# Kernel tuning notes

Measured on AMD Instinct MI355X. Metric: run time of the kernel, lower is better.

Reference implementation:

```python
import jax, jax.numpy as jnp
import numpy as np

NORMALIZED_LENGTH = 1.0
LOSS_WEIGHTS = (0.25, 1.0)
EPS = 1e-12  # matches torch F.normalize eps


def setup_inputs() -> dict:
    key = jax.random.key(0)
    k1, k2 = jax.random.split(key)
    x = jax.random.normal(k1, (16, 128, 64, 64), dtype=jnp.float32)
    codebook = jax.random.normal(k2, (1024, 128), dtype=jnp.float32)
    return {"x": x, "codebook": codebook}


def _forward(x, codebook):
    # --- VQCodebook.forward: normalize x along channel dim (dim=1) ---
    # NOTE: the torch source's codebook renormalization uses non-in-place
    # .div/.mul whose results are discarded, so the codebook is unchanged.
    if NORMALIZED_LENGTH > 0:
        nrm = jnp.linalg.norm(x, axis=1, keepdims=True)  # [B,1,H,W]
        x = NORMALIZED_LENGTH * x / jnp.maximum(nrm, EPS)

    B, C, H, W = x.shape
    z = jnp.transpose(x, (0, 2, 3, 1)).reshape(-1, C)  # [N, C], N = B*H*W

    # Pairwise squared L2 distances via ||z||^2 - 2 z c^T + ||c||^2.
    # argmin of squared distance == argmin of distance.
    z2 = jnp.sum(z * z, axis=1, keepdims=True)             # [N, 1]
    c2 = jnp.sum(codebook * codebook, axis=1)              # [K]
    d2 = z2 - 2.0 * jnp.einsum('nc,kc->nk', z, codebook) + c2[None, :]  # [N, K]
    idx = jnp.argmin(d2, axis=1)                           # [N]

    q = codebook[idx]                                      # [N, C]
    q = q.reshape(B, H, W, C).transpose(0, 3, 1, 2)        # [B, C, H, W]

    lw0, lw1 = LOSS_WEIGHTS
    diff_codebook = jax.lax.stop_gradient(x) - q
    diff_commit = x - jax.lax.stop_gradient(q)
    loss0 = lw0 * jnp.mean(jnp.linalg.norm(diff_codebook, axis=1))
    loss1 = lw1 * jnp.mean(jnp.linalg.norm(diff_commit, axis=1))
    return q, loss0, loss1


def reference(x, codebook):
    return _forward(x, codebook)
```

## Files before the change

### kernel.cpp

```cpp
#include <hip/hip_runtime.h>
#include <math.h>

#define K_CODES 1024
#define C_DIM   128
#define HW      4096
#define CHW     (C_DIM*HW)
#define N_POS   65536
#define Q_ELEMS 8388608

#define WS_S    0
#define WS_C2   256
#define WS_IDX  8192


typedef __attribute__((ext_vector_type(8))) short short8;
typedef __attribute__((ext_vector_type(4))) float f32x4;

__device__ __forceinline__ unsigned short f2bf(float f) {
    unsigned u = __float_as_uint(f);
    u += 0x7FFFu + ((u >> 16) & 1u);
    return (unsigned short)(u >> 16);
}

__device__ __forceinline__ void gll16(const void* g, void* l) {
    __builtin_amdgcn_global_load_lds(
        (const __attribute__((address_space(1))) void*)g,
        (__attribute__((address_space(3))) void*)l, 16, 0, 0);
}

__global__ void prep_kernel(const float* __restrict__ cb, float* __restrict__ ws,
                            unsigned short* __restrict__ cbbf) {
    __shared__ __align__(16) unsigned short srow[128];
    int k = blockIdx.x;
    int l = threadIdx.x;
    if (k == 0 && l == 0) *(float*)((char*)ws + WS_S) = 0.f;
    float v1 = cb[k * C_DIM + l];
    float v2 = cb[k * C_DIM + 64 + l];
    int c1 = l, c2 = 64 + l;
    srow[(((c1 >> 3) ^ (k & 7)) << 3) | (c1 & 7)] = f2bf(v1);
    srow[(((c2 >> 3) ^ (k & 7)) << 3) | (c2 & 7)] = f2bf(v2);
    float ss = v1 * v1 + v2 * v2;
    #pragma unroll
    for (int off = 32; off > 0; off >>= 1) ss += __shfl_down(ss, off);
    if (l == 0) ((float*)((char*)ws + WS_C2))[k] = ss;
    __syncthreads();
    if (l < 16) ((uint4*)cbbf)[k * 16 + l] = ((const uint4*)srow)[l];
}

__global__ __launch_bounds__(256, 2) void vq_mfma(const float* __restrict__ x,
                                                  const float* __restrict__ cb,
                                                  const unsigned short* __restrict__ cbbf,
                                                  const float* __restrict__ c2w,
                                                  int* __restrict__ idxw,
                                                  float* __restrict__ Sw,
                                                  float* __restrict__ out) {
    __shared__ __align__(16) unsigned short cbuf[2 * 1024 * 8];
    __shared__ float mbuf[2][2][16][3];
    __shared__ int ibuf[64];

    const int t  = threadIdx.x;
    const int w  = t >> 6;
    const int kh = w & 1;
    const int pg = w >> 1;
    const int ln = t & 63;
    const int lp = ln & 15;
    const int q  = ln >> 4;
    const int bid = blockIdx.x;
    const int b   = bid >> 6;
    const int s0  = (bid & 63) << 6;

    short8 xf[2][4];
    float  r2v[2];
    {
        float ss[2] = {0.f, 0.f};
        #pragma unroll
        for (int pt = 0; pt < 2; ++pt) {
            const float* xgp = x + b * CHW + s0 + pg * 32 + pt * 16 + lp;
            #pragma unroll
            for (int cs = 0; cs < 4; ++cs) {
                union { short8 v; unsigned short u[8]; } fu;
                #pragma unroll
                for (int j = 0; j < 8; ++j) {
                    float vv = xgp[(32 * cs + 8 * q + j) * HW];
                    ss[pt] = fmaf(vv, vv, ss[pt]);
                    fu.u[j] = f2bf(vv);
                }
                xf[pt][cs] = fu.v;
            }
        }
        #pragma unroll
        for (int pt = 0; pt < 2; ++pt) {
            float s = ss[pt];
            s += __shfl_xor(s, 16);
            s += __shfl_xor(s, 32);
            r2v[pt] = -2.0f / fmaxf(sqrtf(s), 1e-12f);
        }
    }

    const float FMAX = __uint_as_float(0x7F7FFFFFu);
    float m1[2] = {FMAX, FMAX}, m2[2] = {FMAX, FMAX}, m3[2] = {FMAX, FMAX};

    const char* gbase = (const char*)cbbf + (kh * 512) * 256 + (pg * 512 + ln) * 16;
    char* lbase = (char*)cbuf + (kh * 1024 + pg * 512) * 16;

    #pragma unroll
    for (int r = 0; r < 8; ++r)
        gll16(gbase + r * 1024, lbase + r * 1024);
    __syncthreads();

    for (int i = 0; i < 8; ++i) {
        const int k0 = kh * 512 + i * 64;

        f32x4 acc[4][2];
        #pragma unroll
        for (int ct = 0; ct < 4; ++ct)
            #pragma unroll
            for (int pt = 0; pt < 2; ++pt) acc[ct][pt] = 0;

        const unsigned short* cbp = cbuf + kh * 8192;
        #pragma unroll
        for (int cs = 0; cs < 4; ++cs) {
            short8 ah[4];
            #pragma unroll
            for (int ct = 0; ct < 4; ++ct) {
                int g = (16 * ct + lp) * 16 + ((4 * cs + q) ^ (lp & 7));
                ah[ct] = *(const short8*)(cbp + g * 8);
            }
            #pragma unroll
            for (int ct = 0; ct < 4; ++ct)
                #pragma unroll
                for (int pt = 0; pt < 2; ++pt)
                    acc[ct][pt] = __builtin_amdgcn_mfma_f32_16x16x32_bf16(
                        ah[ct], xf[pt][cs], acc[ct][pt], 0, 0, 0);
        }

        #pragma unroll
        for (int ct = 0; ct < 4; ++ct) {
            float4 c2vv = *(const float4*)(c2w + k0 + 16 * ct + 4 * q);
            float c2a[4] = {c2vv.x, c2vv.y, c2vv.z, c2vv.w};
            const int kb0 = k0 + 16 * ct + 4 * q;
            #pragma unroll
            for (int pt = 0; pt < 2; ++pt) {
                #pragma unroll
                for (int reg = 0; reg < 4; ++reg) {
                    float s = fmaf(r2v[pt], acc[ct][pt][reg], c2a[reg]);
                    unsigned pb = (__float_as_uint(s) & 0xFFFFFC00u) |
                                  (unsigned)(kb0 + reg);
                    float u  = __uint_as_float(pb);
                    float t3 = __builtin_amdgcn_fmed3f(m2[pt], m3[pt], u);
                    float t2 = __builtin_amdgcn_fmed3f(m1[pt], m2[pt], u);
                    m1[pt] = fminf(m1[pt], u); m2[pt] = t2; m3[pt] = t3;
                }
            }
        }

        if (i < 7) {
            __syncthreads();
            #pragma unroll
            for (int r = 0; r < 8; ++r)
                gll16(gbase + (i + 1) * 16384 + r * 1024, lbase + r * 1024);
            __syncthreads();
        }
    }

    #pragma unroll
    for (int d = 16; d <= 32; d <<= 1) {
        #pragma unroll
        for (int pt = 0; pt < 2; ++pt) {
            float o1 = __shfl_xor(m1[pt], d), o2 = __shfl_xor(m2[pt], d),
                  o3 = __shfl_xor(m3[pt], d);
            float u, t2, t3;
            u = o1; t3 = __builtin_amdgcn_fmed3f(m2[pt], m3[pt], u);
            t2 = __builtin_amdgcn_fmed3f(m1[pt], m2[pt], u);
            m1[pt] = fminf(m1[pt], u); m2[pt] = t2; m3[pt] = t3;
            u = o2; t3 = __builtin_amdgcn_fmed3f(m2[pt], m3[pt], u);
            t2 = __builtin_amdgcn_fmed3f(m1[pt], m2[pt], u);
            m1[pt] = fminf(m1[pt], u); m2[pt] = t2; m3[pt] = t3;
            u = o3; t3 = __builtin_amdgcn_fmed3f(m2[pt], m3[pt], u);
            t2 = __builtin_amdgcn_fmed3f(m1[pt], m2[pt], u);
            m1[pt] = fminf(m1[pt], u); m2[pt] = t2; m3[pt] = t3;
        }
    }

    if (kh == 1 && ln < 16) {
        #pragma unroll
        for (int pt = 0; pt < 2; ++pt) {
            mbuf[pg][pt][lp][0] = m1[pt];
            mbuf[pg][pt][lp][1] = m2[pt];
            mbuf[pg][pt][lp][2] = m3[pt];
        }
    }
    __syncthreads();

    if (kh == 0) {
        float lsum = 0.f;
        #pragma unroll
        for (int pt = 0; pt < 2; ++pt) {
            #pragma unroll
            for (int c = 0; c < 3; ++c) {
                float u  = mbuf[pg][pt][lp][c];
                float t3 = __builtin_amdgcn_fmed3f(m2[pt], m3[pt], u);
                float t2 = __builtin_amdgcn_fmed3f(m1[pt], m2[pt], u);
                m1[pt] = fminf(m1[pt], u); m2[pt] = t2; m3[pt] = t3;
            }
            int ks[3] = {(int)(__float_as_uint(m1[pt]) & 1023u),
                         (int)(__float_as_uint(m2[pt]) & 1023u),
                         (int)(__float_as_uint(m3[pt]) & 1023u)};

            float xr[32];
            const float* xgp = x + b * CHW + s0 + pg * 32 + pt * 16 + lp;
            #pragma unroll
            for (int cs = 0; cs < 4; ++cs)
                #pragma unroll
                for (int j = 0; j < 8; ++j)
                    xr[cs * 8 + j] = xgp[(32 * cs + 8 * q + j) * HW];

            float dots[3];
            #pragma unroll
            for (int jj = 0; jj < 3; ++jj) {
                const float* crow = cb + ks[jj] * C_DIM + 8 * q;
                float p = 0.f;
                #pragma unroll
                for (int cs = 0; cs < 4; ++cs) {
                    float4 a0 = *(const float4*)(crow + 32 * cs);
                    float4 a1 = *(const float4*)(crow + 32 * cs + 4);
                    p = fmaf(xr[cs*8+0], a0.x, p); p = fmaf(xr[cs*8+1], a0.y, p);
                    p = fmaf(xr[cs*8+2], a0.z, p); p = fmaf(xr[cs*8+3], a0.w, p);
                    p = fmaf(xr[cs*8+4], a1.x, p); p = fmaf(xr[cs*8+5], a1.y, p);
                    p = fmaf(xr[cs*8+6], a1.z, p); p = fmaf(xr[cs*8+7], a1.w, p);
                }
                p += __shfl_xor(p, 16);
                p += __shfl_xor(p, 32);
                dots[jj] = p;
            }
            float sb = fmaf(r2v[pt], dots[0], c2w[ks[0]]); int kb = ks[0];
            float s2 = fmaf(r2v[pt], dots[1], c2w[ks[1]]);
            if (s2 < sb || (s2 == sb && ks[1] < kb)) { sb = s2; kb = ks[1]; }
            float s3 = fmaf(r2v[pt], dots[2], c2w[ks[2]]);
            if (s3 < sb || (s3 == sb && ks[2] < kb)) { sb = s3; kb = ks[2]; }

            if (ln < 16) {
                idxw[bid * 64 + pg * 32 + pt * 16 + lp] = kb;
                ibuf[pg * 32 + pt * 16 + lp] = kb;
            }
            lsum += sqrtf(fmaxf(1.0f + sb, 0.f));
        }
        #pragma unroll
        for (int off = 32; off > 0; off >>= 1) lsum += __shfl_down(lsum, off);
        if (ln == 0) atomicAdd(Sw, 0.25f * lsum);
    }

    __syncthreads();
    if (b != 0) {
        const int row = ibuf[ln];
        const float4* cbr = (const float4*)cb + row * 32;
        float* ob = out + b * CHW + s0 + ln;
        #pragma unroll
        for (int c4 = w * 8; c4 < w * 8 + 8; ++c4) {
            float4 v = cbr[c4];
            float* o = ob + (c4 * 4) * HW;
            o[0]      = v.x;
            o[HW]     = v.y;
            o[2 * HW] = v.z;
            o[3 * HW] = v.w;
        }
    }
}

__global__ void write_q0(const float* __restrict__ cb,
                         const int* __restrict__ idxw,
                         const float* __restrict__ ws,
                         float* __restrict__ out) {
    int id = blockIdx.x * 256 + threadIdx.x;
    int s  = id & 4095;
    int c4 = id >> 12;
    int row = idxw[s];
    float4 v = ((const float4*)cb)[row * 32 + c4];
    float* o = out + (c4 * 4) * HW + s;
    o[0]      = v.x;
    o[HW]     = v.y;
    o[2 * HW] = v.z;
    o[3 * HW] = v.w;
    if (id == 0) {
        float S = *(const float*)((const char*)ws + WS_S);
        float m = S / (float)N_POS;
        out[Q_ELEMS]     = 0.25f * m;
        out[Q_ELEMS + 1] = m;
    }
}

extern "C" void kernel_launch(void* const* d_in, const int* in_sizes, int n_in,
                              void* d_out, int out_size, void* d_ws, size_t ws_size,
                              hipStream_t stream) {
    const float* x  = (const float*)d_in[0];
    const float* cb = (const float*)d_in[1];
    float* out = (float*)d_out;
    float* ws  = (float*)d_ws;

    const float* c2w = (const float*)((const char*)d_ws + WS_C2);
    int*  idxw = (int*)((char*)d_ws + WS_IDX);
    float* Sw  = (float*)((char*)d_ws + WS_S);
    unsigned short* cbbf = (unsigned short*)d_out;

    prep_kernel<<<K_CODES, 64, 0, stream>>>(cb, ws, cbbf);
    vq_mfma    <<<N_POS / 64, 256, 0, stream>>>(x, cb, cbbf, c2w, idxw, Sw, out);
    write_q0   <<<512, 256, 0, stream>>>(cb, idxw, ws, out);
}
```

Measured before the change: 70.66 us.

## Give each wave a private codebook quarter with double-buffered async loads

Each of the four waves now owns a 256-code slice of the codebook and processes all 64 positions, rather than splitting codes in halves and positions in pairs. Each wave streams its slice through its own double-buffered LDS region and synchronises with s_waitcnt alone, so block-wide __syncthreads are gone and the next chunk's load overlaps the current MFMA work. The top-3 merge now reduces candidates from four waves through LDS. The cost is more registers for x fragments and accumulators (4 position tiles per wave), which may reduce occupancy, plus each wave re-reading and converting all of x.

```diff
diff --git a/kernel.cpp b/kernel.cpp
--- a/kernel.cpp
+++ b/kernel.cpp
@@ -54,14 +54,12 @@
                                                   int* __restrict__ idxw,
                                                   float* __restrict__ Sw,
                                                   float* __restrict__ out) {
-    __shared__ __align__(16) unsigned short cbuf[2 * 1024 * 8];
-    __shared__ float mbuf[2][2][16][3];
+    __shared__ __align__(16) unsigned short cbuf[2][4][4096];
+    __shared__ float mbuf[4][4][16][3];
     __shared__ int ibuf[64];
 
     const int t  = threadIdx.x;
     const int w  = t >> 6;
-    const int kh = w & 1;
-    const int pg = w >> 1;
     const int ln = t & 63;
     const int lp = ln & 15;
     const int q  = ln >> 4;
@@ -69,13 +67,23 @@
     const int b   = bid >> 6;
     const int s0  = (bid & 63) << 6;
 
-    short8 xf[2][4];
-    float  r2v[2];
+    const char* gq = (const char*)cbbf + (w << 16);
+
     {
-        float ss[2] = {0.f, 0.f};
-        #pragma unroll
-        for (int pt = 0; pt < 2; ++pt) {
-            const float* xgp = x + b * CHW + s0 + pg * 32 + pt * 16 + lp;
+        const char* gs = gq + (ln << 4);
+        char* ld = (char*)&cbuf[0][w][0];
+        #pragma unroll
+        for (int r = 0; r < 8; ++r) gll16(gs + r * 1024, ld + r * 1024);
+    }
+
+    short8 xf[4][4];
+    float  r2v[4];
+    {
+        float ss[4];
+        #pragma unroll
+        for (int pt = 0; pt < 4; ++pt) {
+            ss[pt] = 0.f;
+            const float* xgp = x + b * CHW + s0 + pt * 16 + lp;
             #pragma unroll
             for (int cs = 0; cs < 4; ++cs) {
                 union { short8 v; unsigned short u[8]; } fu;
@@ -89,7 +97,7 @@
             }
         }
         #pragma unroll
-        for (int pt = 0; pt < 2; ++pt) {
+        for (int pt = 0; pt < 4; ++pt) {
             float s = ss[pt];
             s += __shfl_xor(s, 16);
             s += __shfl_xor(s, 32);
@@ -98,49 +106,54 @@
     }
 
     const float FMAX = __uint_as_float(0x7F7FFFFFu);
-    float m1[2] = {FMAX, FMAX}, m2[2] = {FMAX, FMAX}, m3[2] = {FMAX, FMAX};
-
-    const char* gbase = (const char*)cbbf + (kh * 512) * 256 + (pg * 512 + ln) * 16;
-    char* lbase = (char*)cbuf + (kh * 1024 + pg * 512) * 16;
-
-    #pragma unroll
-    for (int r = 0; r < 8; ++r)
-        gll16(gbase + r * 1024, lbase + r * 1024);
-    __syncthreads();
+    float m1[4] = {FMAX, FMAX, FMAX, FMAX};
+    float m2[4] = {FMAX, FMAX, FMAX, FMAX};
+    float m3[4] = {FMAX, FMAX, FMAX, FMAX};
+
+    asm volatile("s_waitcnt vmcnt(0)" ::: "memory");
+    __builtin_amdgcn_sched_barrier(0);
 
     for (int i = 0; i < 8; ++i) {
-        const int k0 = kh * 512 + i * 64;
-
-        f32x4 acc[4][2];
-        #pragma unroll
-        for (int ct = 0; ct < 4; ++ct)
-            #pragma unroll
-            for (int pt = 0; pt < 2; ++pt) acc[ct][pt] = 0;
-
-        const unsigned short* cbp = cbuf + kh * 8192;
+        if (i < 7) {
+            asm volatile("s_waitcnt lgkmcnt(0)" ::: "memory");
+            const char* gs = gq + (i + 1) * 8192 + (ln << 4);
+            char* ld = (char*)&cbuf[(i + 1) & 1][w][0];
+            #pragma unroll
+            for (int r = 0; r < 8; ++r) gll16(gs + r * 1024, ld + r * 1024);
+        }
+
+        const int k0 = (w << 8) + (i << 5);
+        const unsigned short* cbp = &cbuf[i & 1][w][0];
+
+        f32x4 acc[2][4];
+        #pragma unroll
+        for (int ct = 0; ct < 2; ++ct)
+            #pragma unroll
+            for (int pt = 0; pt < 4; ++pt) acc[ct][pt] = 0;
+
         #pragma unroll
         for (int cs = 0; cs < 4; ++cs) {
-            short8 ah[4];
-            #pragma unroll
-            for (int ct = 0; ct < 4; ++ct) {
+            short8 ah[2];
+            #pragma unroll
+            for (int ct = 0; ct < 2; ++ct) {
                 int g = (16 * ct + lp) * 16 + ((4 * cs + q) ^ (lp & 7));
                 ah[ct] = *(const short8*)(cbp + g * 8);
             }
             #pragma unroll
-            for (int ct = 0; ct < 4; ++ct)
-                #pragma unroll
-                for (int pt = 0; pt < 2; ++pt)
+            for (int ct = 0; ct < 2; ++ct)
+                #pragma unroll
+                for (int pt = 0; pt < 4; ++pt)
                     acc[ct][pt] = __builtin_amdgcn_mfma_f32_16x16x32_bf16(
                         ah[ct], xf[pt][cs], acc[ct][pt], 0, 0, 0);
         }
 
         #pragma unroll
-        for (int ct = 0; ct < 4; ++ct) {
+        for (int ct = 0; ct < 2; ++ct) {
             float4 c2vv = *(const float4*)(c2w + k0 + 16 * ct + 4 * q);
             float c2a[4] = {c2vv.x, c2vv.y, c2vv.z, c2vv.w};
             const int kb0 = k0 + 16 * ct + 4 * q;
             #pragma unroll
-            for (int pt = 0; pt < 2; ++pt) {
+            for (int pt = 0; pt < 4; ++pt) {
                 #pragma unroll
                 for (int reg = 0; reg < 4; ++reg) {
                     float s = fmaf(r2v[pt], acc[ct][pt][reg], c2a[reg]);
@@ -155,18 +168,15 @@
         }
 
         if (i < 7) {
-            __syncthreads();
-            #pragma unroll
-            for (int r = 0; r < 8; ++r)
-                gll16(gbase + (i + 1) * 16384 + r * 1024, lbase + r * 1024);
-            __syncthreads();
+            asm volatile("s_waitcnt vmcnt(0)" ::: "memory");
+            __builtin_amdgcn_sched_barrier(0);
         }
     }
 
     #pragma unroll
     for (int d = 16; d <= 32; d <<= 1) {
         #pragma unroll
-        for (int pt = 0; pt < 2; ++pt) {
+        for (int pt = 0; pt < 4; ++pt) {
             float o1 = __shfl_xor(m1[pt], d), o2 = __shfl_xor(m2[pt], d),
                   o3 = __shfl_xor(m3[pt], d);
             float u, t2, t3;
@@ -182,33 +192,37 @@
         }
     }
 
-    if (kh == 1 && ln < 16) {
-        #pragma unroll
-        for (int pt = 0; pt < 2; ++pt) {
-            mbuf[pg][pt][lp][0] = m1[pt];
-            mbuf[pg][pt][lp][1] = m2[pt];
-            mbuf[pg][pt][lp][2] = m3[pt];
+    if (ln < 16) {
+        #pragma unroll
+        for (int pt = 0; pt < 4; ++pt) {
+            mbuf[w][pt][lp][0] = m1[pt];
+            mbuf[w][pt][lp][1] = m2[pt];
+            mbuf[w][pt][lp][2] = m3[pt];
         }
     }
     __syncthreads();
 
-    if (kh == 0) {
+    if (w < 2) {
         float lsum = 0.f;
         #pragma unroll
-        for (int pt = 0; pt < 2; ++pt) {
-            #pragma unroll
-            for (int c = 0; c < 3; ++c) {
-                float u  = mbuf[pg][pt][lp][c];
-                float t3 = __builtin_amdgcn_fmed3f(m2[pt], m3[pt], u);
-                float t2 = __builtin_amdgcn_fmed3f(m1[pt], m2[pt], u);
-                m1[pt] = fminf(m1[pt], u); m2[pt] = t2; m3[pt] = t3;
-            }
-            int ks[3] = {(int)(__float_as_uint(m1[pt]) & 1023u),
-                         (int)(__float_as_uint(m2[pt]) & 1023u),
-                         (int)(__float_as_uint(m3[pt]) & 1023u)};
+        for (int ptl = 0; ptl < 2; ++ptl) {
+            const int pt = 2 * w + ptl;
+            float M1 = FMAX, M2 = FMAX, M3 = FMAX;
+            #pragma unroll
+            for (int ww = 0; ww < 4; ++ww)
+                #pragma unroll
+                for (int c = 0; c < 3; ++c) {
+                    float u  = mbuf[ww][pt][lp][c];
+                    float t3 = __builtin_amdgcn_fmed3f(M2, M3, u);
+                    float t2 = __builtin_amdgcn_fmed3f(M1, M2, u);
+                    M1 = fminf(M1, u); M2 = t2; M3 = t3;
+                }
+            int ks[3] = {(int)(__float_as_uint(M1) & 1023u),
+                         (int)(__float_as_uint(M2) & 1023u),
+                         (int)(__float_as_uint(M3) & 1023u)};
 
             float xr[32];
-            const float* xgp = x + b * CHW + s0 + pg * 32 + pt * 16 + lp;
+            const float* xgp = x + b * CHW + s0 + pt * 16 + lp;
             #pragma unroll
             for (int cs = 0; cs < 4; ++cs)
                 #pragma unroll
@@ -240,8 +254,8 @@
             if (s3 < sb || (s3 == sb && ks[2] < kb)) { sb = s3; kb = ks[2]; }
 
             if (ln < 16) {
-                idxw[bid * 64 + pg * 32 + pt * 16 + lp] = kb;
-                ibuf[pg * 32 + pt * 16 + lp] = kb;
+                idxw[bid * 64 + pt * 16 + lp] = kb;
+                ibuf[pt * 16 + lp] = kb;
             }
             lsum += sqrtf(fmaxf(1.0f + sb, 0.f));
         }
```

Result: faster. 68.39 us (median of 2 runs) (-3.2%).
